# Optimization experiments

Hardware: AMD Instinct MI355X
Metric: run time of the kernel (lower is better)

## Reference

```python
import jax, jax.numpy as jnp
import numpy as np
import math

B, L, CIN = 16, 1024, 14
T = 256            # num_tokens
H = 2 * T          # S4 channel width
N = 32             # S4 state size (d_state)
E = 128            # embedding_dim
DEPTH = 6
BETA0, BETA1 = 1e-4, 2e-2


def conv1x1(W, b, x):
    # W: [O, C], b: [O], x: [B, C, L] -> [B, O, L]
    return jnp.einsum('oc,bcl->bol', W, x) + b[None, :, None]


def layernorm_c(x, g, b):
    # normalize over channel dim of [B, C, L]
    mu = jnp.mean(x, axis=1, keepdims=True)
    var = jnp.mean((x - mu) ** 2, axis=1, keepdims=True)
    return (x - mu) * jax.lax.rsqrt(var + 1e-5) * g[None, :, None] + b[None, :, None]


def s4d(u, log_dt, logA_re, A_im, C_re, C_im, D):
    # Standard S4D: diagonal SSM, ZOH-ish discretization, FFT depthwise conv.
    # u: [B, H, L]
    Lq = u.shape[-1]
    dt = jnp.exp(log_dt)                       # [H]
    A = -jnp.exp(logA_re) + 1j * A_im          # [H, N]
    dtA = A * dt[:, None]                      # [H, N]
    C = (C_re + 1j * C_im) * (jnp.exp(dtA) - 1.0) / A
    V = jnp.exp(dtA[:, :, None] * jnp.arange(Lq, dtype=jnp.float32))  # [H, N, L]
    K = 2.0 * jnp.einsum('hn,hnl->hl', C, V).real                    # [H, L]
    nfft = 2 * Lq
    y = jnp.fft.irfft(jnp.fft.rfft(u, n=nfft) * jnp.fft.rfft(K, n=nfft)[None], n=nfft)[..., :Lq]
    return y + D[None, :, None] * u


def setup_inputs() -> dict:
    key = jax.random.key(0)
    ks = iter(jax.random.split(key, 64))
    nrm = lambda shape, s=1.0: jax.random.normal(next(ks), shape, jnp.float32) * s
    inp = {}
    inp['x'] = nrm((B, L, CIN))
    inp['t'] = jax.random.uniform(next(ks), (B,), jnp.float32, 1e-3, 1.0)
    # diffusion embedding
    inp['gfp_W'] = nrm((E // 2,), 30.0)
    inp['emb_w1'] = nrm((E, E), E ** -0.5); inp['emb_b1'] = jnp.zeros((E,), jnp.float32)
    inp['emb_w2'] = nrm((E, E), E ** -0.5); inp['emb_b2'] = jnp.zeros((E,), jnp.float32)
    # top-level projections
    inp['in_w'] = nrm((T, CIN), CIN ** -0.5); inp['in_b'] = jnp.zeros((T,), jnp.float32)
    inp['out1_w'] = nrm((T, T), T ** -0.5); inp['out1_b'] = jnp.zeros((T,), jnp.float32)
    inp['out2_w'] = nrm((CIN, T), T ** -0.5); inp['out2_b'] = jnp.zeros((CIN,), jnp.float32)
    # per-block params (stacked over depth)
    inp['dp_w'] = nrm((DEPTH, T, E), E ** -0.5); inp['dp_b'] = jnp.zeros((DEPTH, T), jnp.float32)
    inp['ip_w'] = nrm((DEPTH, H, T), T ** -0.5); inp['ip_b'] = jnp.zeros((DEPTH, H), jnp.float32)
    inp['op_w'] = nrm((DEPTH, H, T), T ** -0.5); inp['op_b'] = jnp.zeros((DEPTH, H), jnp.float32)
    # S4D params: [DEPTH, 2, H, ...] (two S4 layers per block)
    lo, hi = math.log(1e-3), math.log(1e-1)
    inp['s4_log_dt'] = jax.random.uniform(next(ks), (DEPTH, 2, H), jnp.float32, lo, hi)
    inp['s4_logA_re'] = jnp.full((DEPTH, 2, H, N), math.log(0.5), jnp.float32)
    inp['s4_A_im'] = jnp.broadcast_to(math.pi * jnp.arange(N, dtype=jnp.float32), (DEPTH, 2, H, N)).copy()
    inp['s4_C_re'] = nrm((DEPTH, 2, H, N), 0.5 ** 0.5)
    inp['s4_C_im'] = nrm((DEPTH, 2, H, N), 0.5 ** 0.5)
    inp['s4_D'] = nrm((DEPTH, 2, H))
    inp['ln_g'] = jnp.ones((DEPTH, 2, H), jnp.float32)
    inp['ln_b'] = jnp.zeros((DEPTH, 2, H), jnp.float32)
    return inp


def reference(x, t, gfp_W, emb_w1, emb_b1, emb_w2, emb_b2, in_w, in_b,
              out1_w, out1_b, out2_w, out2_b, dp_w, dp_b, ip_w, ip_b,
              op_w, op_b, s4_log_dt, s4_logA_re, s4_A_im, s4_C_re, s4_C_im,
              s4_D, ln_g, ln_b):
    xt = jnp.swapaxes(x, -1, -2)  # [B, CIN, L]
    # Gaussian Fourier projection + MLP (SiLU)
    xp = t[:, None] * gfp_W[None, :] * (2.0 * math.pi)
    emb = jnp.concatenate([jnp.sin(xp), jnp.cos(xp)], axis=-1)        # [B, E]
    emb = jax.nn.silu(emb @ emb_w1.T + emb_b1)
    emb = jax.nn.silu(emb @ emb_w2.T + emb_b2)
    h = conv1x1(in_w, in_b, xt)                                       # [B, T, L]
    skip_sum = jnp.zeros_like(h)
    for d in range(DEPTH):
        y = h + (emb @ dp_w[d].T + dp_b[d])[:, :, None]
        y = conv1x1(ip_w[d], ip_b[d], y)                              # [B, H, L]
        y = s4d(y, s4_log_dt[d, 0], s4_logA_re[d, 0], s4_A_im[d, 0], s4_C_re[d, 0], s4_C_im[d, 0], s4_D[d, 0])
        y = layernorm_c(y, ln_g[d, 0], ln_b[d, 0])
        y = s4d(y, s4_log_dt[d, 1], s4_logA_re[d, 1], s4_A_im[d, 1], s4_C_re[d, 1], s4_C_im[d, 1], s4_D[d, 1])
        y = layernorm_c(y, ln_g[d, 1], ln_b[d, 1])
        gate, filt = jnp.split(y, 2, axis=1)
        y = jax.nn.sigmoid(gate) * jnp.tanh(filt)                     # [B, T, L]
        y = conv1x1(op_w[d], op_b[d], y)                              # [B, H, L]
        res, skip = jnp.split(y, 2, axis=1)
        h = (h + res) / math.sqrt(2.0)
        skip_sum = skip_sum + skip
    z = skip_sum / math.sqrt(float(DEPTH))
    z = jax.nn.relu(conv1x1(out1_w, out1_b, z))
    z = conv1x1(out2_w, out2_b, z)                                    # [B, CIN, L]
    beta = BETA0 + t * (BETA1 - BETA0)                                # linear schedule
    z = z / jnp.sqrt(beta)[:, None, None]
    return jnp.swapaxes(z, -1, -2)                                    # [B, L, CIN]
```

## Files before the change

### kernel.cpp

```cpp
#include <hip/hip_runtime.h>

#define BB     16
#define LLEN   1024
#define CINN   14
#define TSZ    256
#define HSZ    512
#define NST    32
#define ESZ    128
#define NDEPTH 6
#define QHN    (HSZ*NST)

#define RS2 0.70710678118654752f
#define IS6 0.40824829046386302f

typedef unsigned short u16;
typedef unsigned int   u32;
typedef _Float16 f16;
typedef __attribute__((ext_vector_type(2)))  _Float16 f16x2;
typedef __attribute__((ext_vector_type(4)))  _Float16 f16x4;
typedef __attribute__((ext_vector_type(8)))  _Float16 f16x8;
typedef __attribute__((ext_vector_type(16))) float    f32x16;

#define OFF_LAM   0u
#define OFF_C     393216u
#define OFF_LAMP  786432u
#define OFF_EMB   1179648u
#define OFF_DPE16 1181696u
#define OFF_H     1193984u
#define OFF_Y16   5388288u
#define OFF_HT    9582592u
#define OFF_GT    11679744u
#define OFF_ST    13776896u
#define OFF_ZT    15874048u
#define OFF_MEAN  17971200u
#define OFF_RSTD  17987584u
#define OFF_MATS  18003968u
#define WS_FLOATS 55752704u

#define MATS_PER_LAYER ((size_t)512*12288)

__global__ void consts_kernel(const float* __restrict__ log_dt, const float* __restrict__ logA,
                              const float* __restrict__ Aim,   const float* __restrict__ Cre,
                              const float* __restrict__ Cim,
                              float2* __restrict__ lam2, float2* __restrict__ C2,
                              float2* __restrict__ lamP){
  int gid = blockIdx.x*256 + threadIdx.x;
  int h = (gid>>5) & 511;
  int q = gid >> 14;
  float dt  = expf(log_dt[q*HSZ + h]);
  float are = -expf(logA[gid]);
  float aim = Aim[gid];
  float dre = are*dt, dim = aim*dt;
  float e   = expf(dre);
  float lre = e*cosf(dim), lim = e*sinf(dim);
  float nre = lre - 1.f, nim = lim;
  float invden = 1.f/(are*are + aim*aim);
  float tre = (nre*are + nim*aim)*invden;
  float tim = (nim*are - nre*aim)*invden;
  float cr = Cre[gid], ci = Cim[gid];
  float Cr = 2.f*(cr*tre - ci*tim);
  float Ci = 2.f*(cr*tim + ci*tre);
  lam2[gid] = make_float2(lre, lim);
  C2[gid]   = make_float2(Cr, Ci);
  float pr = lre, pi = lim;
#pragma unroll
  for (int i=0;i<6;i++){ float nr2 = pr*pr - pi*pi; pi = 2.f*pr*pi; pr = nr2; }
  lamP[gid] = make_float2(pr, pi);
}

__global__ __launch_bounds__(256) void build_mats(const float2* __restrict__ lam2d,
                                                  const float2* __restrict__ C2d,
                                                  const float* __restrict__ Dd,
                                                  f16* __restrict__ mats){
  __shared__ float Pre[65][33];
  __shared__ float Pim[65][33];
  __shared__ float Kk[64];
  int bid = blockIdx.x;
  int q   = bid >> 9;
  int h   = bid & 511;
  const float2* lp = lam2d + (size_t)q*QHN + h*NST;
  const float2* cp = C2d  + (size_t)q*QHN + h*NST;
  int tid = threadIdx.x;
  int n  = tid & 31;
  int pg = tid >> 5;
  {
    float2 l = lp[n];
    float ar=l.x, ai=l.y;
#pragma unroll
    for (int i=0;i<3;i++){ float t2 = ar*ar - ai*ai; ai = 2.f*ar*ai; ar = t2; }
    float br=1.f, bi=0.f;
    for (int i=0;i<pg;i++){ float t2 = br*ar - bi*ai; bi = br*ai + bi*ar; br = t2; }
    float pr=br, pi=bi;
#pragma unroll
    for (int i=0;i<8;i++){
      Pre[8*pg+i][n] = pr; Pim[8*pg+i][n] = pi;
      float t2 = pr*l.x - pi*l.y; pi = pr*l.y + pi*l.x; pr = t2;
    }
    if (pg == 7){ Pre[64][n] = pr; Pim[64][n] = pi; }
  }
  __syncthreads();
  if (tid < 64){
    float s = 0.f;
    for (int n2=0;n2<32;n2++){
      float2 c_ = cp[n2];
      s += c_.x*Pre[tid][n2] - c_.y*Pim[tid][n2];
    }
    Kk[tid] = s;
  }
  __syncthreads();
  float Kdiag = Kk[0] + Dd[q*HSZ + h];
  f16* base = mats + (size_t)bid*12288;
#pragma unroll
  for (int jj=0; jj<6; jj++){
    int job = jj*256 + tid;
    int mat = job >> 9;
    int rem = job & 511;
    int m = rem >> 3;
    int g = rem & 7;
    f16x8 vals;
    if (mat == 0){
#pragma unroll
      for (int j8=0;j8<8;j8++){
        int k = g*8 + j8;
        float v = (m > k) ? Kk[m-k] : ((m == k) ? Kdiag : 0.f);
        vals[j8] = (f16)v;
      }
    } else if (mat == 1){
      int n2 = m >> 1; int im = m & 1;
#pragma unroll
      for (int j8=0;j8<8;j8++){
        int k = g*8 + j8; int p = 63 - k;
        vals[j8] = (f16)(im ? Pim[p][n2] : Pre[p][n2]);
      }
    } else {
#pragma unroll
      for (int j8=0;j8<8;j8++){
        int k = g*8 + j8; int n2 = k >> 1;
        float2 c_ = cp[n2];
        float pr = Pre[m+1][n2], pi = Pim[m+1][n2];
        float re  = c_.x*pr - c_.y*pi;
        float imv = c_.x*pi + c_.y*pr;
        vals[j8] = (f16)((k & 1) ? -imv : re);
      }
    }
    *(f16x8*)(base + mat*4096 + (g*64 + m)*8) = vals;
  }
}

__global__ void emb_kernel(const float* __restrict__ t, const float* __restrict__ gw,
                           const float* __restrict__ w1, const float* __restrict__ b1,
                           const float* __restrict__ w2, const float* __restrict__ b2,
                           float* __restrict__ emb){
  __shared__ float e0[128], e1[128];
  int b = blockIdx.x, tid = threadIdx.x;
  float tb = t[b];
  if (tid < 64){
    float xp = tb * gw[tid] * 6.283185307179586f;
    e0[tid]    = sinf(xp);
    e0[tid+64] = cosf(xp);
  }
  __syncthreads();
  float a = b1[tid];
  for (int i=0;i<128;i++) a = fmaf(e0[i], w1[tid*128+i], a);
  a = a / (1.f + __expf(-a));
  e1[tid] = a;
  __syncthreads();
  float a2 = b2[tid];
  for (int i=0;i<128;i++) a2 = fmaf(e1[i], w2[tid*128+i], a2);
  a2 = a2 / (1.f + __expf(-a2));
  emb[b*ESZ + tid] = a2;
}

__global__ void dpe_kernel(const float* __restrict__ emb, const float* __restrict__ dw,
                           const float* __restrict__ db, f16* __restrict__ dpe16){
  int blk = blockIdx.x; int d = blk >> 4; int b = blk & 15; int o = threadIdx.x;
  const float* wp = dw + (size_t)(d*TSZ + o)*ESZ;
  const float* ep = emb + b*ESZ;
  float a = db[d*TSZ + o];
  for (int e=0;e<128;e++) a = fmaf(ep[e], wp[e], a);
  dpe16[(size_t)(d*BB + b)*TSZ + o] = (f16)a;
}

__global__ __launch_bounds__(256) void inproj_kernel(const float* __restrict__ x, const float* __restrict__ w,
                                                     const float* __restrict__ bias, float* __restrict__ hb){
  __shared__ float ws[256*14];
  __shared__ float bs[256];
  int tid = threadIdx.x;
#pragma unroll
  for (int c=0;c<14;c++) ws[tid*14+c] = w[tid*14+c];
  bs[tid] = bias[tid];
  __syncthreads();
  int b = blockIdx.x >> 2;
  int l = ((blockIdx.x & 3) << 8) + tid;
  float xv[14];
  const float* xp = x + (size_t)(b*LLEN + l)*CINN;
#pragma unroll
  for (int c=0;c<14;c++) xv[c] = xp[c];
  for (int o=0;o<256;o++){
    float a = bs[o];
#pragma unroll
    for (int c=0;c<14;c++) a = fmaf(ws[o*14+c], xv[c], a);
    hb[(size_t)(b*TSZ + o)*LLEN + l] = a;
  }
}

__global__ __launch_bounds__(256) void h2t_kernel(const float* __restrict__ src, f16* __restrict__ dst){
  __shared__ f16 TT[64*72];
  int tid = threadIdx.x;
  int b = blockIdx.z;
  int l0 = blockIdx.x * 64;
  int t0 = blockIdx.y * 64;
#pragma unroll
  for (int i=0;i<4;i++){
    int job = i*256 + tid;
    int tt = job >> 4, l4 = (job & 15)*4;
    float4 v = *(const float4*)(src + ((size_t)b*TSZ + t0+tt)*LLEN + l0 + l4);
    TT[(l4+0)*72 + tt] = (f16)v.x;
    TT[(l4+1)*72 + tt] = (f16)v.y;
    TT[(l4+2)*72 + tt] = (f16)v.z;
    TT[(l4+3)*72 + tt] = (f16)v.w;
  }
  __syncthreads();
#pragma unroll
  for (int i=0;i<2;i++){
    int job = i*256 + tid;
    int l = job >> 3, g = job & 7;
    f16x8 hv = *(const f16x8*)(TT + l*72 + g*8);
    *(f16x8*)(dst + ((size_t)b*LLEN + l0 + l)*TSZ + t0 + g*8) = hv;
  }
}

template<int MODE>
__global__ __launch_bounds__(256) void gemm_k(const float* __restrict__ W, const float* __restrict__ bias,
                                              const f16* __restrict__ XT, const f16* __restrict__ dpeD,
                                              f16* __restrict__ Y16o,
                                              f16* __restrict__ hT16, f16* __restrict__ sT16, int first){
  __shared__ f16 sm[17408];
  f16* As = sm;
  f16* Bs = sm + 8192;
  int tid = threadIdx.x;
  int lane = tid & 63;
  int wv = tid >> 6;
  int n_blk = blockIdx.x * 128;
  int m_blk = blockIdx.y * 128;
  int bz = blockIdx.z;
  const f16* Xb = XT + (size_t)bz * (LLEN*TSZ);
  int wm = (wv & 1) * 64;
  int wn = (wv >> 1) * 64;

  f32x16 acc[2][2];
#pragma unroll
  for (int mi=0;mi<2;mi++)
#pragma unroll
    for (int ni=0;ni<2;ni++)
#pragma unroll
      for (int r=0;r<16;r++) acc[mi][ni][r] = 0.f;

  for (int kt=0; kt<4; kt++){
    int k0 = kt*64;
#pragma unroll
    for (int i=0;i<4;i++){
      int job = i*256 + tid;
      int m = job >> 3, gk = job & 7;
      const float* wp = W + (size_t)(m_blk + m)*TSZ + k0 + gk*8;
      float4 u0 = *(const float4*)wp;
      float4 u1 = *(const float4*)(wp+4);
      f16x8 hv;
      hv[0]=(f16)u0.x; hv[1]=(f16)u0.y; hv[2]=(f16)u0.z; hv[3]=(f16)u0.w;
      hv[4]=(f16)u1.x; hv[5]=(f16)u1.y; hv[6]=(f16)u1.z; hv[7]=(f16)u1.w;
      int P = m*8 + (gk ^ (m & 7));
      *(f16x8*)(As + P*8) = hv;
    }
#pragma unroll
    for (int i=0;i<4;i++){
      int job = i*256 + tid;
      int n = job >> 3, gk = job & 7;
      f16x8 hv = *(const f16x8*)(Xb + (size_t)(n_blk + n)*TSZ + k0 + gk*8);
      if (MODE==0){
        f16x8 dv = *(const f16x8*)(dpeD + bz*TSZ + k0 + gk*8);
#pragma unroll
        for (int e=0;e<8;e++) hv[e] = hv[e] + dv[e];
      }
      if (MODE==2){
#pragma unroll
        for (int e=0;e<8;e++) hv[e] = hv[e] * (f16)IS6;
      }
      int P = n*8 + (gk ^ (n & 7));
      *(f16x8*)(Bs + P*8) = hv;
    }
    __syncthreads();
#pragma unroll
    for (int ks=0; ks<4; ks++){
      int q = lane >> 5;
      int gk = ks*2 + q;
      f16x8 af[2], bf[2];
#pragma unroll
      for (int mi=0; mi<2; mi++){
        int m = wm + mi*32 + (lane & 31);
        af[mi] = *(const f16x8*)(As + (m*8 + (gk ^ (m&7)))*8);
      }
#pragma unroll
      for (int ni=0; ni<2; ni++){
        int n = wn + ni*32 + (lane & 31);
        bf[ni] = *(const f16x8*)(Bs + (n*8 + (gk ^ (n&7)))*8);
      }
#pragma unroll
      for (int mi=0; mi<2; mi++)
#pragma unroll
        for (int ni=0; ni<2; ni++)
          acc[mi][ni] = __builtin_amdgcn_mfma_f32_32x32x16_f16(af[mi], bf[ni], acc[mi][ni], 0, 0, 0);
    }
    __syncthreads();
  }

  int q = lane >> 5;
  if (MODE == 0){
#pragma unroll
    for (int mi=0;mi<2;mi++)
#pragma unroll
      for (int ni=0;ni<2;ni++){
        int col = n_blk + wn + ni*32 + (lane & 31);
#pragma unroll
        for (int r=0;r<16;r++){
          int row = m_blk + wm + mi*32 + (r&3) + 8*(r>>2) + 4*q;
          float v = acc[mi][ni][r] + bias[row];
          Y16o[((size_t)bz*HSZ + row)*LLEN + col] = (f16)v;
        }
      }
  } else if (MODE == 2){
#pragma unroll
    for (int mi=0;mi<2;mi++)
#pragma unroll
      for (int ni=0;ni<2;ni++){
        int col_l = wn + ni*32 + (lane & 31);
#pragma unroll
        for (int r=0;r<16;r++){
          int row_l = wm + mi*32 + (r&3) + 8*(r>>2) + 4*q;
          float v = fmaxf(acc[mi][ni][r] + bias[m_blk + row_l], 0.f);
          sm[col_l*136 + row_l] = (f16)v;
        }
      }
    __syncthreads();
#pragma unroll
    for (int i=0;i<8;i++){
      int job = i*256 + tid;
      int n = job >> 4, m8 = job & 15;
      f16x8 hv = *(const f16x8*)(sm + n*136 + m8*8);
      *(f16x8*)(Y16o + ((size_t)bz*LLEN + n_blk + n)*TSZ + m_blk + m8*8) = hv;
    }
  } else {
    int isRes = (blockIdx.y < 2);
    f16* dst = isRes ? hT16 : sT16;
    int mOff  = isRes ? m_blk : (m_blk - TSZ);
    int doLoad = isRes || !first;
    if (doLoad){
#pragma unroll
      for (int i=0;i<8;i++){
        int job = i*256 + tid;
        int n = job >> 4, m8 = job & 15;
        f16x8 hv = *(const f16x8*)(dst + ((size_t)bz*LLEN + n_blk + n)*TSZ + mOff + m8*8);
        *(f16x8*)(sm + n*136 + m8*8) = hv;
      }
      __syncthreads();
    }
#pragma unroll
    for (int mi=0;mi<2;mi++)
#pragma unroll
      for (int ni=0;ni<2;ni++){
        int col_l = wn + ni*32 + (lane & 31);
#pragma unroll
        for (int r=0;r<16;r++){
          int row_l = wm + mi*32 + (r&3) + 8*(r>>2) + 4*q;
          float v = acc[mi][ni][r] + bias[m_blk + row_l];
          if (isRes){
            float old = (float)sm[col_l*136 + row_l];
            sm[col_l*136 + row_l] = (f16)((old + v)*RS2);
          } else if (first){
            sm[col_l*136 + row_l] = (f16)v;
          } else {
            float old = (float)sm[col_l*136 + row_l];
            sm[col_l*136 + row_l] = (f16)(old + v);
          }
        }
      }
    __syncthreads();
#pragma unroll
    for (int i=0;i<8;i++){
      int job = i*256 + tid;
      int n = job >> 4, m8 = job & 15;
      f16x8 hv = *(const f16x8*)(sm + n*136 + m8*8);
      *(f16x8*)(dst + ((size_t)bz*LLEN + n_blk + n)*TSZ + mOff + m8*8) = hv;
    }
  }
}

template<int LN>
__global__ __launch_bounds__(128) void s4_mfma(const f16* __restrict__ matsq,
                                               const float2* __restrict__ lamPq,
                                               const f16* u, f16* y,
                                               const float* __restrict__ meanp,
                                               const float* __restrict__ rstdp,
                                               const float* __restrict__ gp,
                                               const float* __restrict__ btp){
  __shared__ f16 Ubuf[64*72];
  __shared__ f16 ZSbuf[64*72];

  int tid  = threadIdx.x;
  int w    = tid >> 6;
  int lane = tid & 63;
  int q    = lane >> 5;
  int colL = lane & 31;
  int h  = blockIdx.x & 511;
  int bq = blockIdx.x >> 9;
  int b0 = bq*4;

  float gv = 0.f, bv = 0.f;
  if (LN){ gv = gp[h]; bv = btp[h]; }

  const f16* matT = matsq + (size_t)h*12288;
  const f16* matV = matT + 4096;
  const f16* matE = matT + 8192;

#pragma unroll
  for (int i=0;i<4;i++){
    int fidx = i*64 + lane;
    int row = fidx >> 7;
    int l   = (fidx & 127)*8;
    int b   = b0 + 2*w + row;
    f16x8 hv = *(const f16x8*)(u + ((size_t)b*HSZ + h)*LLEN + l);
    if (LN){
      float4 m0 = *(const float4*)(meanp + b*LLEN + l);
      float4 m1 = *(const float4*)(meanp + b*LLEN + l + 4);
      float4 r0 = *(const float4*)(rstdp + b*LLEN + l);
      float4 r1 = *(const float4*)(rstdp + b*LLEN + l + 4);
      float mm[8] = {m0.x,m0.y,m0.z,m0.w,m1.x,m1.y,m1.z,m1.w};
      float rr[8] = {r0.x,r0.y,r0.z,r0.w,r1.x,r1.y,r1.z,r1.w};
#pragma unroll
      for (int e=0;e<8;e++)
        hv[e] = (f16)(((float)hv[e] - mm[e])*rr[e]*gv + bv);
    }
    int col = (2*w + row)*16 + (l >> 6);
    *(f16x8*)(Ubuf + col*72 + (l & 63)) = hv;
  }
  __syncthreads();

  int strip = w*32;

  {
    f32x16 zacc[2];
#pragma unroll
    for (int mt=0;mt<2;mt++)
#pragma unroll
      for (int r=0;r<16;r++) zacc[mt][r] = 0.f;
#pragma unroll
    for (int kt=0; kt<4; kt++){
      int kg = kt*2 + q;
      f16x8 bfrag = *(const f16x8*)(Ubuf + (strip+colL)*72 + kg*8);
#pragma unroll
      for (int mt=0; mt<2; mt++){
        f16x8 afrag = *(const f16x8*)(matV + ((size_t)(kg*64 + mt*32 + colL))*8);
        zacc[mt] = __builtin_amdgcn_mfma_f32_32x32x16_f16(afrag, bfrag, zacc[mt], 0, 0, 0);
      }
    }
#pragma unroll
    for (int mt=0;mt<2;mt++)
#pragma unroll
      for (int rg=0;rg<4;rg++){
        int st0 = mt*32 + rg*8 + q*4;
        f16x4 zp;
        zp[0]=(f16)zacc[mt][rg*4+0]; zp[1]=(f16)zacc[mt][rg*4+1];
        zp[2]=(f16)zacc[mt][rg*4+2]; zp[3]=(f16)zacc[mt][rg*4+3];
        *(f16x4*)(ZSbuf + (strip+colL)*72 + st0) = zp;
      }
  }
  __syncthreads();

  {
    int n  = lane & 31;
    int colb = (2*w + (lane>>5))*16;
    float2 l64 = lamPq[h*NST + n];
    float Sre = 0.f, Sim = 0.f;
#pragma unroll
    for (int c=0;c<16;c++){
      f16* p = ZSbuf + (colb + c)*72 + 2*n;
      f16x2 z2 = *(f16x2*)p;
      f16x2 sp_; sp_[0] = (f16)Sre; sp_[1] = (f16)Sim;
      *(f16x2*)p = sp_;
      float nr = fmaf(l64.x, Sre, fmaf(-l64.y, Sim, (float)z2[0]));
      float ni = fmaf(l64.x, Sim, fmaf( l64.y, Sre, (float)z2[1]));
      Sre = nr; Sim = ni;
    }
  }
  __syncthreads();

  f32x16 yacc[2];
#pragma unroll
  for (int mt=0;mt<2;mt++)
#pragma unroll
    for (int r=0;r<16;r++) yacc[mt][r] = 0.f;
#pragma unroll
  for (int kt=0; kt<4; kt++){
    int kg = kt*2 + q;
    f16x8 bu = *(const f16x8*)(Ubuf  + (strip+colL)*72 + kg*8);
    f16x8 bs = *(const f16x8*)(ZSbuf + (strip+colL)*72 + kg*8);
#pragma unroll
    for (int mt=0; mt<2; mt++){
      f16x8 aT = *(const f16x8*)(matT + ((size_t)(kg*64 + mt*32 + colL))*8);
      yacc[mt] = __builtin_amdgcn_mfma_f32_32x32x16_f16(aT, bu, yacc[mt], 0, 0, 0);
    }
#pragma unroll
    for (int mt=0; mt<2; mt++){
      f16x8 aE = *(const f16x8*)(matE + ((size_t)(kg*64 + mt*32 + colL))*8);
      yacc[mt] = __builtin_amdgcn_mfma_f32_32x32x16_f16(aE, bs, yacc[mt], 0, 0, 0);
    }
  }
  __syncthreads();

#pragma unroll
  for (int mt=0;mt<2;mt++)
#pragma unroll
    for (int rg=0;rg<4;rg++){
      int j0 = mt*32 + rg*8 + q*4;
      f16x4 yv;
      yv[0]=(f16)yacc[mt][rg*4+0]; yv[1]=(f16)yacc[mt][rg*4+1];
      yv[2]=(f16)yacc[mt][rg*4+2]; yv[3]=(f16)yacc[mt][rg*4+3];
      *(f16x4*)(ZSbuf + (strip+colL)*72 + j0) = yv;
    }
  __syncthreads();
#pragma unroll
  for (int i=0;i<4;i++){
    int fidx = i*64 + lane;
    int row = fidx >> 7;
    int l   = (fidx & 127)*8;
    int b   = b0 + 2*w + row;
    int col = (2*w + row)*16 + (l >> 6);
    f16x8 hv = *(const f16x8*)(ZSbuf + col*72 + (l & 63));
    *(f16x8*)(y + ((size_t)b*HSZ + h)*LLEN + l) = hv;
  }
}

__global__ __launch_bounds__(256) void ln_stats(const f16* __restrict__ in,
                                                float* __restrict__ mean, float* __restrict__ rstd){
  __shared__ float rs[8][32];
  __shared__ float rq[8][32];
  int tid = threadIdx.x;
  int hg = tid >> 5;
  int lo = tid & 31;
  int b = blockIdx.x >> 5;
  int l = ((blockIdx.x & 31) << 5) + lo;
  size_t base = (size_t)(b*HSZ)*LLEN + l;
  float s=0.f, ss=0.f;
  for (int hh=0; hh<64; hh++){
    float v = (float)in[base + (size_t)(hg*64+hh)*LLEN];
    s += v; ss = fmaf(v,v,ss);
  }
  rs[hg][lo]=s; rq[hg][lo]=ss;
  __syncthreads();
  if (tid < 32){
    float S=0.f, Q=0.f;
#pragma unroll
    for (int g=0; g<8; g++){ S += rs[g][tid]; Q += rq[g][tid]; }
    float mn = S * (1.f/HSZ);
    float var  = Q * (1.f/HSZ) - mn*mn;
    int lw = ((blockIdx.x & 31) << 5) + tid;
    mean[b*LLEN + lw] = mn;
    rstd[b*LLEN + lw] = rsqrtf(var + 1e-5f);
  }
}

__global__ __launch_bounds__(256) void ln_gate_kernel(const f16* __restrict__ in, f16* __restrict__ gT,
                                                      const float* __restrict__ g, const float* __restrict__ bt){
  __shared__ float rs[8][32];
  __shared__ float rq[8][32];
  __shared__ float mbuf[32], rbuf[32];
  __shared__ f16 gbuf[32*272];
  int tid = threadIdx.x;
  int hg = tid >> 5;
  int lo = tid & 31;
  int b = blockIdx.x >> 5;
  int l0 = (blockIdx.x & 31) << 5;
  int l = l0 + lo;
  size_t base = (size_t)(b*HSZ)*LLEN + l;
  float s=0.f, ss=0.f;
  for (int hh=0; hh<64; hh++){
    float v = (float)in[base + (size_t)(hg*64+hh)*LLEN];
    s += v; ss = fmaf(v,v,ss);
  }
  rs[hg][lo]=s; rq[hg][lo]=ss;
  __syncthreads();
  if (tid < 32){
    float S=0.f, Q=0.f;
#pragma unroll
    for (int gg=0; gg<8; gg++){ S += rs[gg][tid]; Q += rq[gg][tid]; }
    float mean = S * (1.f/HSZ);
    float var  = Q * (1.f/HSZ) - mean*mean;
    mbuf[tid]=mean;
    rbuf[tid]=rsqrtf(var + 1e-5f);
  }
  __syncthreads();
  float mean = mbuf[lo], rstd = rbuf[lo];
  for (int tt=0; tt<32; tt++){
    int t = hg*32 + tt;
    float a = ((float)in[base + (size_t)t*LLEN]       - mean)*rstd*g[t]     + bt[t];
    float f = ((float)in[base + (size_t)(t+256)*LLEN] - mean)*rstd*g[t+256] + bt[t+256];
    float sg = 1.f/(1.f+__expf(-a));
    float th = 1.f - 2.f/(__expf(2.f*f)+1.f);
    gbuf[lo*272 + t] = (f16)(sg*th);
  }
  __syncthreads();
#pragma unroll
  for (int i=0;i<4;i++){
    int job = i*256 + tid;
    int ll = job >> 5, g8 = (job & 31)*8;
    f16x8 hv = *(const f16x8*)(gbuf + ll*272 + g8);
    *(f16x8*)(gT + ((size_t)b*LLEN + l0 + ll)*TSZ + g8) = hv;
  }
}

__global__ __launch_bounds__(256) void out2_kernel(const float* __restrict__ w2, const float* __restrict__ b2,
                                                   const float* __restrict__ t, const f16* __restrict__ zT,
                                                   float* __restrict__ outp){
  __shared__ f16 zt[64*264];
  __shared__ float wsm[14*256];
  __shared__ float part[64][4][16];
  __shared__ float bs[14];
  int tid = threadIdx.x;
#pragma unroll
  for (int c=0;c<14;c++) wsm[c*256+tid] = w2[c*256+tid];
  if (tid < 14) bs[tid] = b2[tid];
  int b = blockIdx.x >> 4;
  int l0 = (blockIdx.x & 15) * 64;
#pragma unroll
  for (int i=0;i<8;i++){
    int job = i*256 + tid;
    int ll = job >> 5, g8 = (job & 31)*8;
    f16x8 hv = *(const f16x8*)(zT + ((size_t)b*LLEN + l0 + ll)*TSZ + g8);
    *(f16x8*)(zt + ll*264 + g8) = hv;
  }
  __syncthreads();
  int l = tid >> 2;
  int g = tid & 3;
  float acc[14];
#pragma unroll
  for (int c=0;c<14;c++) acc[c]=0.f;
  for (int k=0;k<64;k++){
    float zv = (float)zt[l*264 + g*64 + k];
#pragma unroll
    for (int c=0;c<14;c++) acc[c] = fmaf(wsm[c*256 + g*64 + k], zv, acc[c]);
  }
#pragma unroll
  for (int c=0;c<14;c++) part[l][g][c] = acc[c];
  __syncthreads();
  if (g == 0){
    float tb = t[b];
    float scale = rsqrtf(1e-4f + tb*(2e-2f - 1e-4f));
    float* op = outp + (size_t)(b*LLEN + l0 + l)*CINN;
#pragma unroll
    for (int c=0;c<14;c++)
      op[c] = (part[l][0][c]+part[l][1][c]+part[l][2][c]+part[l][3][c] + bs[c])*scale;
  }
}

extern "C" void kernel_launch(void* const* d_in, const int* in_sizes, int n_in,
                              void* d_out, int out_size, void* d_ws, size_t ws_size,
                              hipStream_t stream) {
  (void)in_sizes; (void)n_in; (void)out_size;
  if (ws_size < (size_t)WS_FLOATS * 4) return;

  const float* x      = (const float*)d_in[0];
  const float* t      = (const float*)d_in[1];
  const float* gfpW   = (const float*)d_in[2];
  const float* ew1    = (const float*)d_in[3];
  const float* eb1    = (const float*)d_in[4];
  const float* ew2    = (const float*)d_in[5];
  const float* eb2    = (const float*)d_in[6];
  const float* in_w   = (const float*)d_in[7];
  const float* in_b   = (const float*)d_in[8];
  const float* out1_w = (const float*)d_in[9];
  const float* out1_b = (const float*)d_in[10];
  const float* out2_w = (const float*)d_in[11];
  const float* out2_b = (const float*)d_in[12];
  const float* dp_w   = (const float*)d_in[13];
  const float* dp_b   = (const float*)d_in[14];
  const float* ip_w   = (const float*)d_in[15];
  const float* ip_b   = (const float*)d_in[16];
  const float* op_w   = (const float*)d_in[17];
  const float* op_b   = (const float*)d_in[18];
  const float* log_dt = (const float*)d_in[19];
  const float* logA   = (const float*)d_in[20];
  const float* Aim    = (const float*)d_in[21];
  const float* Cre    = (const float*)d_in[22];
  const float* Cim    = (const float*)d_in[23];
  const float* s4D    = (const float*)d_in[24];
  const float* ln_g   = (const float*)d_in[25];
  const float* ln_b   = (const float*)d_in[26];
  float* out = (float*)d_out;
  float* ws = (float*)d_ws;

  float2* lam2  = (float2*)(ws + OFF_LAM);
  float2* C2v   = (float2*)(ws + OFF_C);
  float2* lamP  = (float2*)(ws + OFF_LAMP);
  float* embb  = ws + OFF_EMB;
  f16*   dpe16 = (f16*)(ws + OFF_DPE16);
  float* hbuf  = ws + OFF_H;
  f16*   y16   = (f16*)(ws + OFF_Y16);
  f16*   hT16  = (f16*)(ws + OFF_HT);
  f16*   gT16  = (f16*)(ws + OFF_GT);
  f16*   sT16  = (f16*)(ws + OFF_ST);
  f16*   zT16  = (f16*)(ws + OFF_ZT);
  float* meanb = ws + OFF_MEAN;
  float* rstdb = ws + OFF_RSTD;
  f16*   mats  = (f16*)(ws + OFF_MATS);

  consts_kernel<<<768,256,0,stream>>>(log_dt, logA, Aim, Cre, Cim, lam2, C2v, lamP);
  build_mats<<<6144,256,0,stream>>>(lam2, C2v, s4D, mats);
  emb_kernel<<<BB,128,0,stream>>>(t, gfpW, ew1, eb1, ew2, eb2, embb);
  dpe_kernel<<<NDEPTH*BB,256,0,stream>>>(embb, dp_w, dp_b, dpe16);
  inproj_kernel<<<64,256,0,stream>>>(x, in_w, in_b, hbuf);
  h2t_kernel<<<dim3(16,4,16),256,0,stream>>>(hbuf, hT16);

  for (int d=0; d<NDEPTH; d++){
    int q0 = d*2, q1 = d*2+1;
    gemm_k<0><<<dim3(8,4,16),256,0,stream>>>(ip_w + (size_t)d*HSZ*TSZ, ip_b + d*HSZ,
                                             hT16, dpe16 + (size_t)d*BB*TSZ,
                                             y16, nullptr, nullptr, 0);
    s4_mfma<0><<<2048,128,0,stream>>>(mats + (size_t)q0*MATS_PER_LAYER, lamP + (size_t)q0*QHN,
                                      y16, y16, nullptr, nullptr, nullptr, nullptr);
    ln_stats<<<512,256,0,stream>>>(y16, meanb, rstdb);
    s4_mfma<1><<<2048,128,0,stream>>>(mats + (size_t)q1*MATS_PER_LAYER, lamP + (size_t)q1*QHN,
                                      y16, y16, meanb, rstdb, ln_g + q0*HSZ, ln_b + q0*HSZ);
    ln_gate_kernel<<<512,256,0,stream>>>(y16, gT16, ln_g + q1*HSZ, ln_b + q1*HSZ);
    gemm_k<1><<<dim3(8,4,16),256,0,stream>>>(op_w + (size_t)d*HSZ*TSZ, op_b + d*HSZ,
                                             gT16, nullptr, nullptr, hT16, sT16, (d==0)?1:0);
  }
  gemm_k<2><<<dim3(8,2,16),256,0,stream>>>(out1_w, out1_b, sT16, nullptr,
                                           zT16, nullptr, nullptr, 0);
  out2_kernel<<<256,256,0,stream>>>(out2_w, out2_b, t, zT16, out);
}
```

Baseline: 731.6 us.

## Fuse embedding/dpe and inproj/transpose kernels; vectorize layernorm reductions

Merges the timestep embedding MLP and the per-depth projection into a single kernel. Each block recomputes the small MLP, so those redundant FLOPs replace one launch and a global round trip. The input projection now writes the transposed f16 hidden state directly through shared memory, which removes the fp32 intermediate buffer and a separate transpose kernel, and it runs 256 blocks instead of 64. The ln_stats and ln_gate kernels switch to 8-wide f16 vector loads along L with wave shuffle reductions, replacing strided scalar loads. This is meant to cut memory transactions in kernels that run every layer.

After: 709.7 us. 3.0% less time.

```diff
diff --git a/kernel.cpp b/kernel.cpp
--- a/kernel.cpp
+++ b/kernel.cpp
@@ -24,9 +24,7 @@
 #define OFF_LAM   0u
 #define OFF_C     393216u
 #define OFF_LAMP  786432u
-#define OFF_EMB   1179648u
 #define OFF_DPE16 1181696u
-#define OFF_H     1193984u
 #define OFF_Y16   5388288u
 #define OFF_HT    9582592u
 #define OFF_GT    11679744u
@@ -147,12 +145,15 @@
   }
 }
 
-__global__ void emb_kernel(const float* __restrict__ t, const float* __restrict__ gw,
-                           const float* __restrict__ w1, const float* __restrict__ b1,
-                           const float* __restrict__ w2, const float* __restrict__ b2,
-                           float* __restrict__ emb){
-  __shared__ float e0[128], e1[128];
-  int b = blockIdx.x, tid = threadIdx.x;
+__global__ __launch_bounds__(256) void embdpe_kernel(const float* __restrict__ t, const float* __restrict__ gw,
+                                                     const float* __restrict__ w1, const float* __restrict__ b1,
+                                                     const float* __restrict__ w2, const float* __restrict__ b2,
+                                                     const float* __restrict__ dw, const float* __restrict__ db,
+                                                     f16* __restrict__ dpe16){
+  __shared__ float e0[128], e1[128], e2[128];
+  int bid = blockIdx.x;
+  int d = bid >> 4, b = bid & 15;
+  int tid = threadIdx.x;
   float tb = t[b];
   if (tid < 64){
     float xp = tb * gw[tid] * 6.283185307179586f;
@@ -160,73 +161,56 @@
     e0[tid+64] = cosf(xp);
   }
   __syncthreads();
-  float a = b1[tid];
-  for (int i=0;i<128;i++) a = fmaf(e0[i], w1[tid*128+i], a);
-  a = a / (1.f + __expf(-a));
-  e1[tid] = a;
-  __syncthreads();
-  float a2 = b2[tid];
-  for (int i=0;i<128;i++) a2 = fmaf(e1[i], w2[tid*128+i], a2);
-  a2 = a2 / (1.f + __expf(-a2));
-  emb[b*ESZ + tid] = a2;
-}
-
-__global__ void dpe_kernel(const float* __restrict__ emb, const float* __restrict__ dw,
-                           const float* __restrict__ db, f16* __restrict__ dpe16){
-  int blk = blockIdx.x; int d = blk >> 4; int b = blk & 15; int o = threadIdx.x;
+  if (tid < 128){
+    float a = b1[tid];
+    for (int i=0;i<128;i++) a = fmaf(e0[i], w1[tid*128+i], a);
+    e1[tid] = a / (1.f + __expf(-a));
+  }
+  __syncthreads();
+  if (tid < 128){
+    float a2 = b2[tid];
+    for (int i=0;i<128;i++) a2 = fmaf(e1[i], w2[tid*128+i], a2);
+    e2[tid] = a2 / (1.f + __expf(-a2));
+  }
+  __syncthreads();
+  int o = tid;
   const float* wp = dw + (size_t)(d*TSZ + o)*ESZ;
-  const float* ep = emb + b*ESZ;
   float a = db[d*TSZ + o];
-  for (int e=0;e<128;e++) a = fmaf(ep[e], wp[e], a);
+  for (int e=0;e<128;e++) a = fmaf(e2[e], wp[e], a);
   dpe16[(size_t)(d*BB + b)*TSZ + o] = (f16)a;
 }
 
-__global__ __launch_bounds__(256) void inproj_kernel(const float* __restrict__ x, const float* __restrict__ w,
-                                                     const float* __restrict__ bias, float* __restrict__ hb){
+__global__ __launch_bounds__(256) void inproj_t_kernel(const float* __restrict__ x, const float* __restrict__ w,
+                                                       const float* __restrict__ bias, f16* __restrict__ hT){
   __shared__ float ws[256*14];
   __shared__ float bs[256];
+  __shared__ f16 TT[64*264];
   int tid = threadIdx.x;
 #pragma unroll
   for (int c=0;c<14;c++) ws[tid*14+c] = w[tid*14+c];
   bs[tid] = bias[tid];
   __syncthreads();
-  int b = blockIdx.x >> 2;
-  int l = ((blockIdx.x & 3) << 8) + tid;
+  int b  = blockIdx.x >> 4;
+  int l0 = (blockIdx.x & 15) * 64;
+  int ll = tid & 63;
+  int tq = tid >> 6;
   float xv[14];
-  const float* xp = x + (size_t)(b*LLEN + l)*CINN;
+  const float* xp = x + (size_t)(b*LLEN + l0 + ll)*CINN;
 #pragma unroll
   for (int c=0;c<14;c++) xv[c] = xp[c];
-  for (int o=0;o<256;o++){
-    float a = bs[o];
-#pragma unroll
-    for (int c=0;c<14;c++) a = fmaf(ws[o*14+c], xv[c], a);
-    hb[(size_t)(b*TSZ + o)*LLEN + l] = a;
-  }
-}
-
-__global__ __launch_bounds__(256) void h2t_kernel(const float* __restrict__ src, f16* __restrict__ dst){
-  __shared__ f16 TT[64*72];
-  int tid = threadIdx.x;
-  int b = blockIdx.z;
-  int l0 = blockIdx.x * 64;
-  int t0 = blockIdx.y * 64;
-#pragma unroll
-  for (int i=0;i<4;i++){
+  for (int tt=tq*64; tt<tq*64+64; tt++){
+    float a = bs[tt];
+#pragma unroll
+    for (int c=0;c<14;c++) a = fmaf(ws[tt*14+c], xv[c], a);
+    TT[ll*264 + tt] = (f16)a;
+  }
+  __syncthreads();
+#pragma unroll
+  for (int i=0;i<8;i++){
     int job = i*256 + tid;
-    int tt = job >> 4, l4 = (job & 15)*4;
-    float4 v = *(const float4*)(src + ((size_t)b*TSZ + t0+tt)*LLEN + l0 + l4);
-    TT[(l4+0)*72 + tt] = (f16)v.x;
-    TT[(l4+1)*72 + tt] = (f16)v.y;
-    TT[(l4+2)*72 + tt] = (f16)v.z;
-    TT[(l4+3)*72 + tt] = (f16)v.w;
-  }
-  __syncthreads();
-#pragma unroll
-  for (int i=0;i<2;i++){
-    int job = i*256 + tid;
-    int l = job >> 3, g = job & 7;
-    f16x8 hv = *(const f16x8*)(TT + l*72 + g*8);
-    *(f16x8*)(dst + ((size_t)b*LLEN + l0 + l)*TSZ + t0 + g*8) = hv;
+    int l2 = job >> 5, g8 = (job & 31)*8;
+    f16x8 hv = *(const f16x8*)(TT + l2*264 + g8);
+    *(f16x8*)(hT + ((size_t)b*LLEN + l0 + l2)*TSZ + g8) = hv;
   }
 }
 
@@ -541,78 +525,135 @@
 
 __global__ __launch_bounds__(256) void ln_stats(const f16* __restrict__ in,
                                                 float* __restrict__ mean, float* __restrict__ rstd){
-  __shared__ float rs[8][32];
-  __shared__ float rq[8][32];
+  __shared__ float rs[4][32];
+  __shared__ float rq[4][32];
   int tid = threadIdx.x;
-  int hg = tid >> 5;
-  int lo = tid & 31;
-  int b = blockIdx.x >> 5;
-  int l = ((blockIdx.x & 31) << 5) + lo;
-  size_t base = (size_t)(b*HSZ)*LLEN + l;
-  float s=0.f, ss=0.f;
-  for (int hh=0; hh<64; hh++){
-    float v = (float)in[base + (size_t)(hg*64+hh)*LLEN];
-    s += v; ss = fmaf(v,v,ss);
-  }
-  rs[hg][lo]=s; rq[hg][lo]=ss;
+  int lg = tid & 3;
+  int hb = tid >> 2;
+  int w  = tid >> 6;
+  int b  = blockIdx.x >> 5;
+  int l0 = (blockIdx.x & 31) << 5;
+  float s8[8], q8[8];
+#pragma unroll
+  for (int j=0;j<8;j++){ s8[j]=0.f; q8[j]=0.f; }
+  const f16* basep = in + (size_t)(b*HSZ)*LLEN + l0 + lg*8;
+#pragma unroll
+  for (int i=0;i<8;i++){
+    int h = hb + 64*i;
+    f16x8 hv = *(const f16x8*)(basep + (size_t)h*LLEN);
+#pragma unroll
+    for (int j=0;j<8;j++){
+      float v = (float)hv[j];
+      s8[j] += v; q8[j] = fmaf(v,v,q8[j]);
+    }
+  }
+#pragma unroll
+  for (int d=4; d<64; d<<=1){
+#pragma unroll
+    for (int j=0;j<8;j++){
+      s8[j] += __shfl_xor(s8[j], (unsigned)d);
+      q8[j] += __shfl_xor(q8[j], (unsigned)d);
+    }
+  }
+  if (((tid>>2) & 15) == 0){
+#pragma unroll
+    for (int j=0;j<8;j++){
+      rs[w][lg*8+j] = s8[j];
+      rq[w][lg*8+j] = q8[j];
+    }
+  }
   __syncthreads();
   if (tid < 32){
-    float S=0.f, Q=0.f;
-#pragma unroll
-    for (int g=0; g<8; g++){ S += rs[g][tid]; Q += rq[g][tid]; }
+    float S = rs[0][tid]+rs[1][tid]+rs[2][tid]+rs[3][tid];
+    float Q = rq[0][tid]+rq[1][tid]+rq[2][tid]+rq[3][tid];
     float mn = S * (1.f/HSZ);
-    float var  = Q * (1.f/HSZ) - mn*mn;
-    int lw = ((blockIdx.x & 31) << 5) + tid;
-    mean[b*LLEN + lw] = mn;
-    rstd[b*LLEN + lw] = rsqrtf(var + 1e-5f);
+    float var = Q * (1.f/HSZ) - mn*mn;
+    mean[b*LLEN + l0 + tid] = mn;
+    rstd[b*LLEN + l0 + tid] = rsqrtf(var + 1e-5f);
   }
 }
 
 __global__ __launch_bounds__(256) void ln_gate_kernel(const f16* __restrict__ in, f16* __restrict__ gT,
                                                       const float* __restrict__ g, const float* __restrict__ bt){
-  __shared__ float rs[8][32];
-  __shared__ float rq[8][32];
+  __shared__ float rs[4][32];
+  __shared__ float rq[4][32];
   __shared__ float mbuf[32], rbuf[32];
-  __shared__ f16 gbuf[32*272];
+  __shared__ f16 gbuf[32*264];
   int tid = threadIdx.x;
-  int hg = tid >> 5;
-  int lo = tid & 31;
-  int b = blockIdx.x >> 5;
+  int lg = tid & 3;
+  int w  = tid >> 6;
+  int b  = blockIdx.x >> 5;
   int l0 = (blockIdx.x & 31) << 5;
-  int l = l0 + lo;
-  size_t base = (size_t)(b*HSZ)*LLEN + l;
-  float s=0.f, ss=0.f;
-  for (int hh=0; hh<64; hh++){
-    float v = (float)in[base + (size_t)(hg*64+hh)*LLEN];
-    s += v; ss = fmaf(v,v,ss);
-  }
-  rs[hg][lo]=s; rq[hg][lo]=ss;
+  {
+    int hb = tid >> 2;
+    float s8[8], q8[8];
+#pragma unroll
+    for (int j=0;j<8;j++){ s8[j]=0.f; q8[j]=0.f; }
+    const f16* basep = in + (size_t)(b*HSZ)*LLEN + l0 + lg*8;
+#pragma unroll
+    for (int i=0;i<8;i++){
+      int h = hb + 64*i;
+      f16x8 hv = *(const f16x8*)(basep + (size_t)h*LLEN);
+#pragma unroll
+      for (int j=0;j<8;j++){
+        float v = (float)hv[j];
+        s8[j] += v; q8[j] = fmaf(v,v,q8[j]);
+      }
+    }
+#pragma unroll
+    for (int d=4; d<64; d<<=1){
+#pragma unroll
+      for (int j=0;j<8;j++){
+        s8[j] += __shfl_xor(s8[j], (unsigned)d);
+        q8[j] += __shfl_xor(q8[j], (unsigned)d);
+      }
+    }
+    if (((tid>>2) & 15) == 0){
+#pragma unroll
+      for (int j=0;j<8;j++){
+        rs[w][lg*8+j] = s8[j];
+        rq[w][lg*8+j] = q8[j];
+      }
+    }
+  }
   __syncthreads();
   if (tid < 32){
-    float S=0.f, Q=0.f;
-#pragma unroll
-    for (int gg=0; gg<8; gg++){ S += rs[gg][tid]; Q += rq[gg][tid]; }
-    float mean = S * (1.f/HSZ);
-    float var  = Q * (1.f/HSZ) - mean*mean;
-    mbuf[tid]=mean;
-    rbuf[tid]=rsqrtf(var + 1e-5f);
-  }
-  __syncthreads();
-  float mean = mbuf[lo], rstd = rbuf[lo];
-  for (int tt=0; tt<32; tt++){
-    int t = hg*32 + tt;
-    float a = ((float)in[base + (size_t)t*LLEN]       - mean)*rstd*g[t]     + bt[t];
-    float f = ((float)in[base + (size_t)(t+256)*LLEN] - mean)*rstd*g[t+256] + bt[t+256];
-    float sg = 1.f/(1.f+__expf(-a));
-    float th = 1.f - 2.f/(__expf(2.f*f)+1.f);
-    gbuf[lo*272 + t] = (f16)(sg*th);
+    float S = rs[0][tid]+rs[1][tid]+rs[2][tid]+rs[3][tid];
+    float Q = rq[0][tid]+rq[1][tid]+rq[2][tid]+rq[3][tid];
+    float mn = S * (1.f/HSZ);
+    float var = Q * (1.f/HSZ) - mn*mn;
+    mbuf[tid] = mn;
+    rbuf[tid] = rsqrtf(var + 1e-5f);
+  }
+  __syncthreads();
+  {
+    int tq = tid >> 2;
+    float mloc[8], rloc[8];
+#pragma unroll
+    for (int j=0;j<8;j++){ mloc[j]=mbuf[lg*8+j]; rloc[j]=rbuf[lg*8+j]; }
+    const f16* basep = in + (size_t)(b*HSZ)*LLEN + l0 + lg*8;
+#pragma unroll
+    for (int i=0;i<4;i++){
+      int t = tq + 64*i;
+      f16x8 av = *(const f16x8*)(basep + (size_t)t*LLEN);
+      f16x8 fv = *(const f16x8*)(basep + (size_t)(t+256)*LLEN);
+      float ga = g[t], ba = bt[t], gf = g[t+256], bf2 = bt[t+256];
+#pragma unroll
+      for (int j=0;j<8;j++){
+        float a = ((float)av[j] - mloc[j])*rloc[j]*ga + ba;
+        float f = ((float)fv[j] - mloc[j])*rloc[j]*gf + bf2;
+        float sg = 1.f/(1.f+__expf(-a));
+        float th = 1.f - 2.f/(__expf(2.f*f)+1.f);
+        gbuf[(lg*8+j)*264 + t] = (f16)(sg*th);
+      }
+    }
   }
   __syncthreads();
 #pragma unroll
   for (int i=0;i<4;i++){
     int job = i*256 + tid;
     int ll = job >> 5, g8 = (job & 31)*8;
-    f16x8 hv = *(const f16x8*)(gbuf + ll*272 + g8);
+    f16x8 hv = *(const f16x8*)(gbuf + ll*264 + g8);
     *(f16x8*)(gT + ((size_t)b*LLEN + l0 + ll)*TSZ + g8) = hv;
   }
 }
@@ -700,9 +741,7 @@
   float2* lam2  = (float2*)(ws + OFF_LAM);
   float2* C2v   = (float2*)(ws + OFF_C);
   float2* lamP  = (float2*)(ws + OFF_LAMP);
-  float* embb  = ws + OFF_EMB;
   f16*   dpe16 = (f16*)(ws + OFF_DPE16);
-  float* hbuf  = ws + OFF_H;
   f16*   y16   = (f16*)(ws + OFF_Y16);
   f16*   hT16  = (f16*)(ws + OFF_HT);
   f16*   gT16  = (f16*)(ws + OFF_GT);
@@ -714,10 +753,8 @@
 
   consts_kernel<<<768,256,0,stream>>>(log_dt, logA, Aim, Cre, Cim, lam2, C2v, lamP);
   build_mats<<<6144,256,0,stream>>>(lam2, C2v, s4D, mats);
-  emb_kernel<<<BB,128,0,stream>>>(t, gfpW, ew1, eb1, ew2, eb2, embb);
-  dpe_kernel<<<NDEPTH*BB,256,0,stream>>>(embb, dp_w, dp_b, dpe16);
-  inproj_kernel<<<64,256,0,stream>>>(x, in_w, in_b, hbuf);
-  h2t_kernel<<<dim3(16,4,16),256,0,stream>>>(hbuf, hT16);
+  embdpe_kernel<<<NDEPTH*BB,256,0,stream>>>(t, gfpW, ew1, eb1, ew2, eb2, dp_w, dp_b, dpe16);
+  inproj_t_kernel<<<256,256,0,stream>>>(x, in_w, in_b, hT16);
 
   for (int d=0; d<NDEPTH; d++){
     int q0 = d*2, q1 = d*2+1;
```
